# Optimization experiments

Measured on AMD Instinct MI355X. Metric: run time of the kernel, lower is better.

Reference implementation:

```python
import jax, jax.numpy as jnp
import numpy as np

NUM_USERS = 100000
NUM_RATINGS = 5
EMBED_DIM = 64
ATT_DIM = 16
B, G, L, S = 16384, 8, 50, 32


def setup_inputs() -> dict:
    key = jax.random.key(0)
    ks = jax.random.split(key, 16)
    inp = {
        # forward args (int / bool constants)
        "nodes": jax.random.randint(ks[0], (B, G), 0, NUM_USERS),
        "history_u": jax.random.randint(ks[1], (B, L), 0, NUM_USERS),
        "history_r": jax.random.randint(ks[2], (B, L), 0, NUM_RATINGS),
        "history_mask": jax.random.randint(ks[3], (B, L), 0, 2).astype(bool).at[:, 0].set(True),
        "social_adj": jax.random.randint(ks[4], (B, S), 0, NUM_USERS),
        "social_mask": jax.random.randint(ks[5], (B, S), 0, 2).astype(bool).at[:, 0].set(True),
        # learned parameters
        "features": jax.random.normal(ks[6], (NUM_USERS, EMBED_DIM), jnp.float32) * 0.02,
        "r_embed": jax.random.normal(ks[7], (NUM_RATINGS, EMBED_DIM), jnp.float32) * 0.02,
        "wg1": jax.random.normal(ks[8], (EMBED_DIM, ATT_DIM), jnp.float32) / np.sqrt(EMBED_DIM),
        "bg1": jnp.zeros((ATT_DIM,), jnp.float32),
        "wg2": jax.random.normal(ks[9], (ATT_DIM, 1), jnp.float32) / np.sqrt(ATT_DIM),
        "bg2": jnp.zeros((1,), jnp.float32),
        "w1": jax.random.normal(ks[10], (2 * EMBED_DIM, EMBED_DIM), jnp.float32) / np.sqrt(2 * EMBED_DIM),
        "b1": jnp.zeros((EMBED_DIM,), jnp.float32),
    }
    return inp


def _masked_mean(x, mask):
    # x: [B, N, D], mask: [B, N] float -> [B, D]
    denom = jnp.maximum(mask.sum(axis=1, keepdims=True), 1.0)
    return (x * mask[..., None]).sum(axis=1) / denom


def reference(nodes, history_u, history_r, history_mask, social_adj, social_mask,
              features, r_embed, wg1, bg1, wg2, bg2, w1, b1):
    dt = features.dtype
    # --- Group_Embedding: attention pooling over member embeddings ---
    members = features[nodes]                              # [B, G, D] gather
    h = jnp.tanh(members @ wg1 + bg1)                      # [B, G, 16]
    logits = (h @ wg2 + bg2)[..., 0]                       # [B, G]
    alpha = jax.nn.softmax(logits, axis=-1)
    self_feats = jnp.einsum('bg,bgd->bd', alpha, members)  # [B, D]

    # --- aggregator: ragged history (item+rating) + social neighbor means ---
    hm = history_mask.astype(dt)
    hist = features[history_u] + r_embed[history_r]        # [B, L, D] gather
    hist_mean = _masked_mean(hist, hm)                     # [B, D]

    sm = social_mask.astype(dt)
    soc_mean = _masked_mean(features[social_adj], sm)      # [B, D]

    neigh_feats = 0.5 * (hist_mean + soc_mean)             # [B, D]

    # --- concat -> linear -> relu ---
    combined = jnp.concatenate([self_feats, neigh_feats], axis=1)  # [B, 2D]
    return jax.nn.relu(combined @ w1 + b1)                 # [B, D]
```

## Files before the change

kernel.cpp:

```cpp
#include <hip/hip_runtime.h>
#include <cstdint>
#include <cstddef>

#define BB 16384

__global__ __launch_bounds__(256) void k_fused(
    const int* __restrict__ nodes, const int* __restrict__ hist_u,
    const int* __restrict__ hist_r, const int* __restrict__ hist_m,
    const int* __restrict__ soc_a, const int* __restrict__ soc_m,
    const float* __restrict__ features, const float* __restrict__ r_embed,
    const float* __restrict__ wg1, const float* __restrict__ bg1,
    const float* __restrict__ wg2, const float* __restrict__ bg2,
    const float* __restrict__ w1, const float* __restrict__ b1,
    float* __restrict__ out)
{
    __shared__ float wg1t[16 * 68];
    __shared__ int   lcomp[4][96];
    __shared__ float scratch[4][272];

    const int tid  = threadIdx.x;
    const int lane = tid & 63;
    const int wv   = tid >> 6;
    const int e    = blockIdx.x * 4 + wv;
    const int sub  = lane & 15;
    const int grp  = lane >> 4;
    const char* fB = (const char*)features;

    {
        const float4 w = ((const float4*)wg1)[tid];
        const int d = tid >> 2, k0 = (tid & 3) * 4;
        wg1t[(k0 + 0) * 68 + d] = w.x;
        wg1t[(k0 + 1) * 68 + d] = w.y;
        wg1t[(k0 + 2) * 68 + d] = w.z;
        wg1t[(k0 + 3) * 68 + d] = w.w;
    }
    __syncthreads();

    lcomp[wv][lane] = 0;
    if (lane < 32) lcomp[wv][64 + lane] = 0;

    int nd = (lane < 8) ? nodes[e * 8 + lane] : 0;
    int hu = 0, hr = 0, hmv = 0;
    if (lane < 50) {
        hu  = hist_u[e * 50 + lane];
        hr  = hist_r[e * 50 + lane];
        hmv = hist_m[e * 50 + lane];
    }
    int sa = 0, sk = 0;
    if (lane < 32) {
        sa = soc_a[e * 32 + lane];
        sk = soc_m[e * 32 + lane];
    }

    const float4* re4p = (const float4*)r_embed;
    const float4 re0 = re4p[0 * 16 + sub];
    const float4 re1 = re4p[1 * 16 + sub];
    const float4 re2 = re4p[2 * 16 + sub];
    const float4 re3 = re4p[3 * 16 + sub];
    const float4 re4 = re4p[4 * 16 + sub];

    uint64_t hb = __ballot(hmv != 0);
    const int hc = (int)__popcll(hb);
    int hrank = (int)__popcll(hb & ((1ull << lane) - 1));

    uint64_t sbm = __ballot(sk != 0);
    const int scn = (int)__popcll(sbm);
    int srank = (int)__popcll(sbm & ((1ull << lane) - 1));

    const float hw = 0.5f / (float)hc;
    const float sw = 0.5f / (float)scn;
    const int   n  = hc + scn;

    if (hmv) lcomp[wv][hrank] = hu << 8;
    if (sk)  lcomp[wv][hc + srank] = sa << 8;

    const int c0 = (int)__popcll(__ballot(hmv && hr == 0));
    const int c1 = (int)__popcll(__ballot(hmv && hr == 1));
    const int c2 = (int)__popcll(__ballot(hmv && hr == 2));
    const int c3 = (int)__popcll(__ballot(hmv && hr == 3));
    const int c4 = (int)__popcll(__ballot(hmv && hr == 4));

    int pkA = lcomp[wv][lane];
    int pkB = lcomp[wv][64 + (lane & 31)];

    const int u0 = __shfl(nd, grp);
    const int u1 = __shfl(nd, 4 + grp);
    const float4 v0 = *(const float4*)(fB + ((unsigned)u0 << 8) + sub * 16);
    const float4 v1 = *(const float4*)(fB + ((unsigned)u1 << 8) + sub * 16);

    const int o0 = __shfl(pkA, 0  + grp);
    const int o1 = __shfl(pkA, 4  + grp);
    const int o2 = __shfl(pkA, 8  + grp);
    const int o3 = __shfl(pkA, 12 + grp);
    const float4 g0 = *(const float4*)(fB + (unsigned)o0 + sub * 16);
    const float4 g1 = *(const float4*)(fB + (unsigned)o1 + sub * 16);
    const float4 g2 = *(const float4*)(fB + (unsigned)o2 + sub * 16);
    const float4 g3 = *(const float4*)(fB + (unsigned)o3 + sub * 16);

    const float bg1v = bg1[sub];
    const float wk2  = wg2[sub];
    float h0 = bg1v, h1 = bg1v;

    *(float4*)&scratch[wv][grp * 68 + sub * 4] = v0;
    #pragma unroll
    for (int d4 = 0; d4 < 16; ++d4) {
        const float4 m  = *(const float4*)&scratch[wv][grp * 68 + d4 * 4];
        const float4 wk = *(const float4*)&wg1t[sub * 68 + d4 * 4];
        h0 += m.x * wk.x + m.y * wk.y + m.z * wk.z + m.w * wk.w;
    }
    *(float4*)&scratch[wv][grp * 68 + sub * 4] = v1;
    #pragma unroll
    for (int d4 = 0; d4 < 16; ++d4) {
        const float4 m  = *(const float4*)&scratch[wv][grp * 68 + d4 * 4];
        const float4 wk = *(const float4*)&wg1t[sub * 68 + d4 * 4];
        h1 += m.x * wk.x + m.y * wk.y + m.z * wk.z + m.w * wk.w;
    }

    {
        float x0 = fminf(fmaxf(h0, -9.f), 9.f);
        float x1 = fminf(fmaxf(h1, -9.f), 9.f);
        float e20 = __expf(2.f * x0), e21 = __expf(2.f * x1);
        h0 = (e20 - 1.f) / (e20 + 1.f) * wk2;
        h1 = (e21 - 1.f) / (e21 + 1.f) * wk2;
        h0 += __shfl_xor(h0, 1); h1 += __shfl_xor(h1, 1);
        h0 += __shfl_xor(h0, 2); h1 += __shfl_xor(h1, 2);
        h0 += __shfl_xor(h0, 4); h1 += __shfl_xor(h1, 4);
        h0 += __shfl_xor(h0, 8); h1 += __shfl_xor(h1, 8);
    }
    const float bg2v = bg2[0];
    const float l0 = h0 + bg2v;
    const float l1 = h1 + bg2v;

    float mx = fmaxf(l0, l1);
    mx = fmaxf(mx, __shfl_xor(mx, 16));
    mx = fmaxf(mx, __shfl_xor(mx, 32));
    float e0 = __expf(l0 - mx), e1 = __expf(l1 - mx);
    float s = e0 + e1;
    s += __shfl_xor(s, 16);
    s += __shfl_xor(s, 32);
    const float a0 = e0 / s, a1 = e1 / s;

    float4 sf4;
    sf4.x = a0 * v0.x + a1 * v1.x;
    sf4.y = a0 * v0.y + a1 * v1.y;
    sf4.z = a0 * v0.z + a1 * v1.z;
    sf4.w = a0 * v0.w + a1 * v1.w;

    float4 nb4 = {0.f, 0.f, 0.f, 0.f};
    {
        const float w0 = (0  + grp < hc) ? hw : ((0  + grp < n) ? sw : 0.f);
        const float w1q= (4  + grp < hc) ? hw : ((4  + grp < n) ? sw : 0.f);
        const float w2 = (8  + grp < hc) ? hw : ((8  + grp < n) ? sw : 0.f);
        const float w3 = (12 + grp < hc) ? hw : ((12 + grp < n) ? sw : 0.f);
        nb4.x += w0 * g0.x + w1q * g1.x + w2 * g2.x + w3 * g3.x;
        nb4.y += w0 * g0.y + w1q * g1.y + w2 * g2.y + w3 * g3.y;
        nb4.z += w0 * g0.z + w1q * g1.z + w2 * g2.z + w3 * g3.z;
        nb4.w += w0 * g0.w + w1q * g1.w + w2 * g2.w + w3 * g3.w;
    }

    for (int base = 16; base < n; base += 16) {
        #pragma unroll
        for (int j = 0; j < 4; ++j) {
            const int cbase = base + j * 4;
            int off;
            if (cbase < 64) off = __shfl(pkA, cbase + grp);
            else            off = __shfl(pkB, cbase - 64 + grp);
            const int idx = cbase + grp;
            const float w = (idx < hc) ? hw : ((idx < n) ? sw : 0.f);
            const float4 v = *(const float4*)(fB + (unsigned)off + sub * 16);
            nb4.x += w * v.x; nb4.y += w * v.y;
            nb4.z += w * v.z; nb4.w += w * v.w;
        }
    }

#define XRED(v4)                                            \
    v4.x += __shfl_xor(v4.x, 16); v4.x += __shfl_xor(v4.x, 32); \
    v4.y += __shfl_xor(v4.y, 16); v4.y += __shfl_xor(v4.y, 32); \
    v4.z += __shfl_xor(v4.z, 16); v4.z += __shfl_xor(v4.z, 32); \
    v4.w += __shfl_xor(v4.w, 16); v4.w += __shfl_xor(v4.w, 32);
    XRED(sf4)
    XRED(nb4)
#undef XRED

    float f0 = hw * (float)c0, f1 = hw * (float)c1, f2 = hw * (float)c2,
          f3 = hw * (float)c3, f4 = hw * (float)c4;
    nb4.x += f0 * re0.x + f1 * re1.x + f2 * re2.x + f3 * re3.x + f4 * re4.x;
    nb4.y += f0 * re0.y + f1 * re1.y + f2 * re2.y + f3 * re3.y + f4 * re4.y;
    nb4.z += f0 * re0.z + f1 * re1.z + f2 * re2.z + f3 * re3.z + f4 * re4.z;
    nb4.w += f0 * re0.w + f1 * re1.w + f2 * re2.w + f3 * re3.w + f4 * re4.w;

    if (grp == 0) *(float4*)&scratch[wv][sub * 4] = sf4;
    if (grp == 1) *(float4*)&scratch[wv][64 + sub * 4] = nb4;

    const int col = lane;
    float y = b1[col];
    #pragma unroll 8
    for (int k4 = 0; k4 < 32; ++k4) {
        const float4 c = *(const float4*)&scratch[wv][k4 * 4];
        y += c.x * w1[(k4 * 4 + 0) * 64 + col]
           + c.y * w1[(k4 * 4 + 1) * 64 + col]
           + c.z * w1[(k4 * 4 + 2) * 64 + col]
           + c.w * w1[(k4 * 4 + 3) * 64 + col];
    }
    out[(size_t)e * 64 + col] = fmaxf(y, 0.f);
}

extern "C" void kernel_launch(void* const* d_in, const int* in_sizes, int n_in,
                              void* d_out, int out_size, void* d_ws, size_t ws_size,
                              hipStream_t stream)
{
    const int*   nodes    = (const int*)d_in[0];
    const int*   hu       = (const int*)d_in[1];
    const int*   hr       = (const int*)d_in[2];
    const int*   hm       = (const int*)d_in[3];
    const int*   sa       = (const int*)d_in[4];
    const int*   smk      = (const int*)d_in[5];
    const float* features = (const float*)d_in[6];
    const float* r_embed  = (const float*)d_in[7];
    const float* wg1      = (const float*)d_in[8];
    const float* bg1      = (const float*)d_in[9];
    const float* wg2      = (const float*)d_in[10];
    const float* bg2      = (const float*)d_in[11];
    const float* w1       = (const float*)d_in[12];
    const float* b1       = (const float*)d_in[13];
    float* out = (float*)d_out;

    (void)d_ws; (void)ws_size;

    k_fused<<<BB / 4, 256, 0, stream>>>(nodes, hu, hr, hm, sa, smk,
                                        features, r_embed, wg1, bg1, wg2, bg2,
                                        w1, b1, out);
}
```

Baseline: 147.4 us.

## Merge LDS buffers, batch member attention, and vectorize final linear layer

```diff
diff --git a/kernel.cpp b/kernel.cpp
--- a/kernel.cpp
+++ b/kernel.cpp
@@ -15,8 +15,7 @@
     float* __restrict__ out)
 {
     __shared__ float wg1t[16 * 68];
-    __shared__ int   lcomp[4][96];
-    __shared__ float scratch[4][272];
+    __shared__ float mrow[4][8 * 68];
 
     const int tid  = threadIdx.x;
     const int lane = tid & 63;
@@ -26,6 +25,9 @@
     const int grp  = lane >> 4;
     const char* fB = (const char*)features;
 
+    int*   lc = (int*)&mrow[wv][0];
+    float* cb = &mrow[wv][0];
+
     {
         const float4 w = ((const float4*)wg1)[tid];
         const int d = tid >> 2, k0 = (tid & 3) * 4;
@@ -34,10 +36,9 @@
         wg1t[(k0 + 2) * 68 + d] = w.z;
         wg1t[(k0 + 3) * 68 + d] = w.w;
     }
-    __syncthreads();
-
-    lcomp[wv][lane] = 0;
-    if (lane < 32) lcomp[wv][64 + lane] = 0;
+
+    lc[lane] = 0;
+    if (lane < 32) lc[64 + lane] = 0;
 
     int nd = (lane < 8) ? nodes[e * 8 + lane] : 0;
     int hu = 0, hr = 0, hmv = 0;
@@ -52,13 +53,6 @@
         sk = soc_m[e * 32 + lane];
     }
 
-    const float4* re4p = (const float4*)r_embed;
-    const float4 re0 = re4p[0 * 16 + sub];
-    const float4 re1 = re4p[1 * 16 + sub];
-    const float4 re2 = re4p[2 * 16 + sub];
-    const float4 re3 = re4p[3 * 16 + sub];
-    const float4 re4 = re4p[4 * 16 + sub];
-
     uint64_t hb = __ballot(hmv != 0);
     const int hc = (int)__popcll(hb);
     int hrank = (int)__popcll(hb & ((1ull << lane) - 1));
@@ -71,8 +65,8 @@
     const float sw = 0.5f / (float)scn;
     const int   n  = hc + scn;
 
-    if (hmv) lcomp[wv][hrank] = hu << 8;
-    if (sk)  lcomp[wv][hc + srank] = sa << 8;
+    if (hmv) lc[hrank] = hu << 8;
+    if (sk)  lc[hc + srank] = sa << 8;
 
     const int c0 = (int)__popcll(__ballot(hmv && hr == 0));
     const int c1 = (int)__popcll(__ballot(hmv && hr == 1));
@@ -80,8 +74,8 @@
     const int c3 = (int)__popcll(__ballot(hmv && hr == 3));
     const int c4 = (int)__popcll(__ballot(hmv && hr == 4));
 
-    int pkA = lcomp[wv][lane];
-    int pkB = lcomp[wv][64 + (lane & 31)];
+    int pkA = lc[lane];
+    int pkB = lc[64 + (lane & 31)];
 
     const int u0 = __shfl(nd, grp);
     const int u1 = __shfl(nd, 4 + grp);
@@ -97,26 +91,24 @@
     const float4 g2 = *(const float4*)(fB + (unsigned)o2 + sub * 16);
     const float4 g3 = *(const float4*)(fB + (unsigned)o3 + sub * 16);
 
-    const float bg1v = bg1[sub];
-    const float wk2  = wg2[sub];
-    float h0 = bg1v, h1 = bg1v;
-
-    *(float4*)&scratch[wv][grp * 68 + sub * 4] = v0;
-    #pragma unroll
-    for (int d4 = 0; d4 < 16; ++d4) {
-        const float4 m  = *(const float4*)&scratch[wv][grp * 68 + d4 * 4];
-        const float4 wk = *(const float4*)&wg1t[sub * 68 + d4 * 4];
-        h0 += m.x * wk.x + m.y * wk.y + m.z * wk.z + m.w * wk.w;
-    }
-    *(float4*)&scratch[wv][grp * 68 + sub * 4] = v1;
-    #pragma unroll
-    for (int d4 = 0; d4 < 16; ++d4) {
-        const float4 m  = *(const float4*)&scratch[wv][grp * 68 + d4 * 4];
-        const float4 wk = *(const float4*)&wg1t[sub * 68 + d4 * 4];
-        h1 += m.x * wk.x + m.y * wk.y + m.z * wk.z + m.w * wk.w;
-    }
-
-    {
+    *(float4*)&mrow[wv][grp * 68 + sub * 4]       = v0;
+    *(float4*)&mrow[wv][(4 + grp) * 68 + sub * 4] = v1;
+
+    __syncthreads();
+
+    float h0, h1;
+    {
+        const float bk = bg1[sub];
+        h0 = bk; h1 = bk;
+        #pragma unroll
+        for (int d4 = 0; d4 < 16; ++d4) {
+            const float4 wk = *(const float4*)&wg1t[sub * 68 + d4 * 4];
+            const float4 m0 = *(const float4*)&mrow[wv][grp * 68 + d4 * 4];
+            const float4 m1 = *(const float4*)&mrow[wv][(4 + grp) * 68 + d4 * 4];
+            h0 += m0.x * wk.x + m0.y * wk.y + m0.z * wk.z + m0.w * wk.w;
+            h1 += m1.x * wk.x + m1.y * wk.y + m1.z * wk.z + m1.w * wk.w;
+        }
+        const float wk2 = wg2[sub];
         float x0 = fminf(fmaxf(h0, -9.f), 9.f);
         float x1 = fminf(fmaxf(h1, -9.f), 9.f);
         float e20 = __expf(2.f * x0), e21 = __expf(2.f * x1);
@@ -182,27 +174,47 @@
     XRED(nb4)
 #undef XRED
 
-    float f0 = hw * (float)c0, f1 = hw * (float)c1, f2 = hw * (float)c2,
-          f3 = hw * (float)c3, f4 = hw * (float)c4;
-    nb4.x += f0 * re0.x + f1 * re1.x + f2 * re2.x + f3 * re3.x + f4 * re4.x;
-    nb4.y += f0 * re0.y + f1 * re1.y + f2 * re2.y + f3 * re3.y + f4 * re4.y;
-    nb4.z += f0 * re0.z + f1 * re1.z + f2 * re2.z + f3 * re3.z + f4 * re4.z;
-    nb4.w += f0 * re0.w + f1 * re1.w + f2 * re2.w + f3 * re3.w + f4 * re4.w;
-
-    if (grp == 0) *(float4*)&scratch[wv][sub * 4] = sf4;
-    if (grp == 1) *(float4*)&scratch[wv][64 + sub * 4] = nb4;
-
-    const int col = lane;
-    float y = b1[col];
+    {
+        const float4* re4p = (const float4*)r_embed;
+        const float4 re0 = re4p[0 * 16 + sub];
+        const float4 re1 = re4p[1 * 16 + sub];
+        const float4 re2 = re4p[2 * 16 + sub];
+        const float4 re3 = re4p[3 * 16 + sub];
+        const float4 re4 = re4p[4 * 16 + sub];
+        float f0 = hw * (float)c0, f1 = hw * (float)c1, f2 = hw * (float)c2,
+              f3 = hw * (float)c3, f4 = hw * (float)c4;
+        nb4.x += f0 * re0.x + f1 * re1.x + f2 * re2.x + f3 * re3.x + f4 * re4.x;
+        nb4.y += f0 * re0.y + f1 * re1.y + f2 * re2.y + f3 * re3.y + f4 * re4.y;
+        nb4.z += f0 * re0.z + f1 * re1.z + f2 * re2.z + f3 * re3.z + f4 * re4.z;
+        nb4.w += f0 * re0.w + f1 * re1.w + f2 * re2.w + f3 * re3.w + f4 * re4.w;
+    }
+
+    if (grp == 0) *(float4*)&cb[sub * 4] = sf4;
+    if (grp == 1) *(float4*)&cb[64 + sub * 4] = nb4;
+
+    float4 p = {0.f, 0.f, 0.f, 0.f};
     #pragma unroll 8
-    for (int k4 = 0; k4 < 32; ++k4) {
-        const float4 c = *(const float4*)&scratch[wv][k4 * 4];
-        y += c.x * w1[(k4 * 4 + 0) * 64 + col]
-           + c.y * w1[(k4 * 4 + 1) * 64 + col]
-           + c.z * w1[(k4 * 4 + 2) * 64 + col]
-           + c.w * w1[(k4 * 4 + 3) * 64 + col];
-    }
-    out[(size_t)e * 64 + col] = fmaxf(y, 0.f);
+    for (int j = 0; j < 32; ++j) {
+        const float  c  = cb[j * 4 + grp];
+        const float4 wv4 = *(const float4*)(w1 + (j * 4 + grp) * 64 + sub * 4);
+        p.x += c * wv4.x;
+        p.y += c * wv4.y;
+        p.z += c * wv4.z;
+        p.w += c * wv4.w;
+    }
+    p.x += __shfl_xor(p.x, 16); p.x += __shfl_xor(p.x, 32);
+    p.y += __shfl_xor(p.y, 16); p.y += __shfl_xor(p.y, 32);
+    p.z += __shfl_xor(p.z, 16); p.z += __shfl_xor(p.z, 32);
+    p.w += __shfl_xor(p.w, 16); p.w += __shfl_xor(p.w, 32);
+    if (grp == 0) {
+        const float4 bv = *(const float4*)(b1 + sub * 4);
+        float4 o;
+        o.x = fmaxf(p.x + bv.x, 0.f);
+        o.y = fmaxf(p.y + bv.y, 0.f);
+        o.z = fmaxf(p.z + bv.z, 0.f);
+        o.w = fmaxf(p.w + bv.w, 0.f);
+        *(float4*)(out + (size_t)e * 64 + sub * 4) = o;
+    }
 }
 
 extern "C" void kernel_launch(void* const* d_in, const int* in_sizes, int n_in,
```

After: 139.6 us. 5.2% less time.
